# Optimization experiments

Measured on AMD Instinct MI355X. Metric: run time of the kernel, lower is better.

Reference implementation:

```python
import jax, jax.numpy as jnp
import numpy as np

H = 0.01          # implicit time step from __init__
KS = 1000.0       # spring stiffness
CG_ITERS = 30     # fixed CG iteration count
EPS = 1e-8


def setup_inputs() -> dict:
    key = jax.random.key(0)
    k1, k2, k3, k4 = jax.random.split(key, 4)
    NV, NE = 200000, 1200000
    rhs = jax.random.normal(k1, (NV, 3), dtype=jnp.float32)
    pos = jax.random.uniform(k2, (NV, 3), dtype=jnp.float32)
    mass = jnp.ones((NV,), dtype=jnp.float32)
    rest_len = jax.random.uniform(k3, (NE,), dtype=jnp.float32) * 0.5 + 0.1
    edges = jax.random.randint(k4, (NE, 2), 0, NV, dtype=jnp.int32)
    return {"rhs": rhs, "pos": pos, "mass": mass, "rest_len": rest_len, "edges": edges}


def _spring_jacobians(pos, edges, rest_len):
    # Per-spring force Jacobian df_i/dx_i for f_i = -ks (|d| - l0) d_hat, d = x_i - x_j
    d = pos[edges[:, 0]] - pos[edges[:, 1]]            # (NE, 3)
    l = jnp.sqrt(jnp.sum(d * d, axis=-1)) + EPS        # (NE,)
    dhat = d / l[:, None]
    ddT = dhat[:, :, None] * dhat[:, None, :]          # (NE, 3, 3)
    I3 = jnp.eye(3, dtype=pos.dtype)
    coef = (1.0 - rest_len / l)[:, None, None]
    Jx = -KS * (coef * (I3 - ddT) + ddT)               # negative semidefinite
    return Jx


def _matvec(v, Jx, e0, e1, mass):
    # A v = M v - h^2 (dF/dx) v, assembled over the spring graph
    dv_e = v[e0] - v[e1]                               # (NE, 3)
    f_e = jnp.einsum('eij,ej->ei', Jx, dv_e)           # (NE, 3)
    Jv = jnp.zeros_like(v).at[e0].add(f_e).at[e1].add(-f_e)
    return mass[:, None] * v - (H * H) * Jv


def reference(rhs, pos, mass, rest_len, edges):
    # Implicit mass-spring step: solve (M - h^2 J) dv = rhs with fixed-iteration CG
    Jx = _spring_jacobians(pos, edges, rest_len)
    e0, e1 = edges[:, 0], edges[:, 1]

    def matvec(v):
        return _matvec(v, Jx, e0, e1, mass)

    b = rhs
    x0 = jnp.zeros_like(b)                             # dv.fill(0.0)
    rs0 = jnp.vdot(b, b)

    def cg_step(carry, _):
        x, r, p, rs = carry
        Ap = matvec(p)
        alpha = rs / (jnp.vdot(p, Ap) + EPS)
        x = x + alpha * p
        r = r - alpha * Ap
        rs_new = jnp.vdot(r, r)
        p = r + (rs_new / (rs + EPS)) * p
        return (x, r, p, rs_new), None

    (x, _, _, _), _ = jax.lax.scan(cg_step, (x0, b, b, rs0), None, length=CG_ITERS)
    return x
```

## Files before the change

kernel.cpp:

```cpp
#include <hip/hip_runtime.h>

#define CG_ITERS 30
#define PAP_OFF 32
#define TILE 8192
#define CHAIN_TB 512
#define ROWSTRIDE 128

__device__ __forceinline__ float fadd32(float a, float b){ return __fadd_rn(a,b); }
__device__ __forceinline__ float fsub32(float a, float b){ return __fsub_rn(a,b); }
__device__ __forceinline__ float fmul32(float a, float b){ return __fmul_rn(a,b); }
__device__ __forceinline__ float fdiv32(float a, float b){ return __fdiv_rn(a,b); }

__device__ __forceinline__ void edge_force(int2 e, int eidx,
                                           const float* __restrict__ pos,
                                           const float* __restrict__ rl,
                                           const float* __restrict__ p,
                                           float f[3]) {
    int i0 = 3 * e.x, i1 = 3 * e.y;
    float d[3], dh[3], dv[3];
    d[0] = fsub32(pos[i0 + 0], pos[i1 + 0]);
    d[1] = fsub32(pos[i0 + 1], pos[i1 + 1]);
    d[2] = fsub32(pos[i0 + 2], pos[i1 + 2]);
    float ss = fadd32(fadd32(fmul32(d[0], d[0]), fmul32(d[1], d[1])), fmul32(d[2], d[2]));
    float l  = fadd32(__fsqrt_rn(ss), 1e-8f);
    dh[0] = fdiv32(d[0], l); dh[1] = fdiv32(d[1], l); dh[2] = fdiv32(d[2], l);
    float coef = fsub32(1.0f, fdiv32(rl[eidx], l));
    dv[0] = fsub32(p[i0 + 0], p[i1 + 0]);
    dv[1] = fsub32(p[i0 + 1], p[i1 + 1]);
    dv[2] = fsub32(p[i0 + 2], p[i1 + 2]);
    #pragma unroll
    for (int i = 0; i < 3; ++i) {
        float acc = 0.0f;
        #pragma unroll
        for (int j = 2; j >= 0; --j) {
            float dd = fmul32(dh[i], dh[j]);
            float t  = (i == j) ? fsub32(1.0f, dd) : fsub32(0.0f, dd);
            float w  = fadd32(fmul32(coef, t), dd);
            float Jx = fmul32(-1000.0f, w);
            acc = fadd32(acc, fmul32(Jx, dv[j]));
        }
        f[i] = acc;
    }
}

__global__ void count_k(const int2* __restrict__ ed, int* __restrict__ cnt0,
                        int* __restrict__ cnt1, int ne) {
    int i = blockIdx.x * blockDim.x + threadIdx.x;
    if (i >= ne) return;
    int2 e = ed[i];
    atomicAdd(&cnt0[e.x], 1);
    atomicAdd(&cnt1[e.y], 1);
}

__global__ void scan_k(const int* __restrict__ cnt0, const int* __restrict__ cnt1,
                       int* __restrict__ segoff, int* __restrict__ split,
                       int* __restrict__ cur0, int* __restrict__ cur1, int nv) {
    __shared__ int lds[1024];
    int tid = threadIdx.x;
    int chunk = (nv + 1023) / 1024;
    int lo = tid * chunk;
    int hi = lo + chunk; if (hi > nv) hi = nv; if (lo > nv) lo = nv;
    int s = 0;
    for (int v = lo; v < hi; ++v) s += cnt0[v] + cnt1[v];
    lds[tid] = s;
    __syncthreads();
    for (int off = 1; off < 1024; off <<= 1) {
        int t = (tid >= off) ? lds[tid - off] : 0;
        __syncthreads();
        lds[tid] += t;
        __syncthreads();
    }
    int run = lds[tid] - s;
    for (int v = lo; v < hi; ++v) {
        int c0 = cnt0[v], c1 = cnt1[v];
        segoff[v] = run;
        split[v]  = run + c0;
        cur0[v]   = run;
        cur1[v]   = run + c0;
        run += c0 + c1;
    }
    if (tid == 1023) segoff[nv] = lds[1023];
}

__global__ void fill_k(const int2* __restrict__ ed, int* __restrict__ cur0,
                       int* __restrict__ cur1, int* __restrict__ inc, int ne) {
    int i = blockIdx.x * blockDim.x + threadIdx.x;
    if (i >= ne) return;
    int2 e = ed[i];
    int s0 = atomicAdd(&cur0[e.x], 1); inc[s0] = i;
    int s1 = atomicAdd(&cur1[e.y], 1); inc[s1] = i;
}

__global__ void sort_k(int* __restrict__ inc, const int* __restrict__ segoff,
                       const int* __restrict__ split, int nv) {
    int v = blockIdx.x * blockDim.x + threadIdx.x;
    if (v >= nv) return;
    int lo = segoff[v], mid = split[v], hi = segoff[v + 1];
    for (int a = lo + 1; a < mid; ++a) {
        int key = inc[a]; int b = a - 1;
        while (b >= lo && inc[b] > key) { inc[b + 1] = inc[b]; --b; }
        inc[b + 1] = key;
    }
    for (int a = mid + 1; a < hi; ++a) {
        int key = inc[a]; int b = a - 1;
        while (b >= mid && inc[b] > key) { inc[b + 1] = inc[b]; --b; }
        inc[b + 1] = key;
    }
}

#define SCHED_FENCE() __builtin_amdgcn_sched_barrier(0)
#define ACC4(v) { s = fadd32(s, (v).x); s = fadd32(s, (v).y); \
                  s = fadd32(s, (v).z); s = fadd32(s, (v).w); }
#define G8_DECL(P) float4 P##0, P##1, P##2, P##3, P##4, P##5, P##6, P##7;
#define G8_LOAD(P, b4, base) { P##0=(b4)[(base)+0]; P##1=(b4)[(base)+1]; \
    P##2=(b4)[(base)+2]; P##3=(b4)[(base)+3]; P##4=(b4)[(base)+4]; \
    P##5=(b4)[(base)+5]; P##6=(b4)[(base)+6]; P##7=(b4)[(base)+7]; }
#define G8_ACC(P) { ACC4(P##0) ACC4(P##1) ACC4(P##2) ACC4(P##3) \
                    ACC4(P##4) ACC4(P##5) ACC4(P##6) ACC4(P##7) }

__device__ __forceinline__ void mark_range(int* __restrict__ tilecnt,
                                           int flo, int fhi) {
    if (fhi <= flo) return;
    __threadfence();
    int t0 = flo / TILE, t1 = (fhi - 1) / TILE;
    for (int t = t0; t <= t1; ++t) {
        int lo = t * TILE;       if (lo < flo) lo = flo;
        int hi = (t + 1) * TILE; if (hi > fhi) hi = fhi;
        atomicAdd(&tilecnt[t], hi - lo);
    }
}

__device__ void chain_consume(const float* __restrict__ prod,
                              int* __restrict__ tilecnt,
                              float* __restrict__ out, int n) {
    __shared__ float buf[2][TILE];
    __shared__ int sgen;
    int tid = threadIdx.x;
    int ntiles = (n + TILE - 1) / TILE;
    if (tid == 0) sgen = -1;
    __syncthreads();

#define WAITSTAGE(T) { \
        int lim = n - (T) * TILE; if (lim > TILE) lim = TILE; \
        if (tid == 64) { \
            while (__hip_atomic_load(&tilecnt[(T)], __ATOMIC_ACQUIRE, \
                                     __HIP_MEMORY_SCOPE_AGENT) < lim) \
                __builtin_amdgcn_s_sleep(1); \
            __hip_atomic_store(&sgen, (T), __ATOMIC_RELEASE, \
                               __HIP_MEMORY_SCOPE_WORKGROUP); \
        } \
        while (__hip_atomic_load(&sgen, __ATOMIC_ACQUIRE, \
                                 __HIP_MEMORY_SCOPE_WORKGROUP) < (T)) \
            __builtin_amdgcn_s_sleep(1); \
        float* dst = buf[(T) & 1]; \
        const float* src = prod + (size_t)(T) * TILE; \
        for (int i = tid - 64; i < lim; i += (CHAIN_TB - 64)) \
            dst[i] = __hip_atomic_load((const float*)&src[i], __ATOMIC_RELAXED, \
                                       __HIP_MEMORY_SCOPE_AGENT); \
    }

    if (tid >= 64) WAITSTAGE(0);
    __syncthreads();
    float s = 0.0f;
    for (int t = 0; t < ntiles; ++t) {
        if (t + 1 < ntiles && tid >= 64) WAITSTAGE(t + 1);
        if (tid == 0) {
            const float* b = buf[t & 1];
            int cfl = n - t * TILE; if (cfl > TILE) cfl = TILE;
            const float4* b4 = (const float4*)b;
            int c4 = cfl >> 2;
            int ng = c4 >> 3;
            int g = 0;
            if (ng >= 5) {
                G8_DECL(A) G8_DECL(B) G8_DECL(C)
                G8_LOAD(A, b4, 0)
                SCHED_FENCE();
                G8_LOAD(B, b4, 8)
                SCHED_FENCE();
                for (; g + 5 <= ng; g += 3) {
                    G8_LOAD(C, b4, (g + 2) << 3)  SCHED_FENCE();
                    G8_ACC(A)                     SCHED_FENCE();
                    G8_LOAD(A, b4, (g + 3) << 3)  SCHED_FENCE();
                    G8_ACC(B)                     SCHED_FENCE();
                    G8_LOAD(B, b4, (g + 4) << 3)  SCHED_FENCE();
                    G8_ACC(C)                     SCHED_FENCE();
                }
                G8_ACC(A)
                G8_ACC(B)
                g += 2;
            }
            for (; g < ng; ++g) {
                G8_DECL(D)
                G8_LOAD(D, b4, g << 3)
                G8_ACC(D)
            }
            for (int i2 = ng << 3; i2 < c4; ++i2) { float4 v = b4[i2]; ACC4(v) }
            for (int k2 = c4 << 2; k2 < cfl; ++k2) s = fadd32(s, b[k2]);
        }
        __syncthreads();
    }
    if (tid == 0) out[0] = s;
#undef WAITSTAGE
}


__global__ void __launch_bounds__(CHAIN_TB, 1)
initchain_k(const float* __restrict__ rhs, float* __restrict__ x,
            float* __restrict__ r, float* __restrict__ p,
            float* __restrict__ prod, int* __restrict__ tilecnt,
            float* __restrict__ out, int n) {
    if (blockIdx.x == 0) { chain_consume(prod, tilecnt, out, n); return; }
    int pb = blockIdx.x - 1;
    int j = pb * CHAIN_TB + threadIdx.x;
    if (j < n) {
        float b = rhs[j];
        x[j] = 0.0f; r[j] = b; p[j] = b;
        prod[j] = fmul32(b, b);
    }
    __syncthreads();
    if (threadIdx.x == 0) {
        int flo = pb * CHAIN_TB;
        int fhi = flo + CHAIN_TB; if (fhi > n) fhi = n;
        mark_range(tilecnt, flo, fhi);
    }
}

__global__ void __launch_bounds__(CHAIN_TB, 1)
mvchain_k(const int2* __restrict__ ed, const float* __restrict__ pos,
          const float* __restrict__ rl, const float* __restrict__ p,
          const float* __restrict__ mass, const int* __restrict__ inc,
          const int* __restrict__ segoff, const int* __restrict__ split,
          float* __restrict__ Ap, float* __restrict__ prod,
          int* __restrict__ tilecnt, float* __restrict__ out,
          int nv, int n3) {
    if (blockIdx.x == 0) { chain_consume(prod, tilecnt, out, n3); return; }
    int pb = blockIdx.x - 1;
    int v = pb * CHAIN_TB + threadIdx.x;
    if (v < nv) {
        int lo = segoff[v], mid = split[v], hi = segoff[v + 1];
        float a0 = 0.0f, a1 = 0.0f, a2 = 0.0f;
        for (int k = lo; k < mid; ++k) {
            int e = inc[k]; float f[3];
            edge_force(ed[e], e, pos, rl, p, f);
            a0 = fadd32(a0, f[0]); a1 = fadd32(a1, f[1]); a2 = fadd32(a2, f[2]);
        }
        for (int k = mid; k < hi; ++k) {
            int e = inc[k]; float f[3];
            edge_force(ed[e], e, pos, rl, p, f);
            a0 = fadd32(a0, -f[0]); a1 = fadd32(a1, -f[1]); a2 = fadd32(a2, -f[2]);
        }
        const float h2 = (float)(0.01 * 0.01);
        int j = 3 * v; float m = mass[v];
        float p0 = p[j], p1 = p[j + 1], p2 = p[j + 2];
        float A0 = fsub32(fmul32(m, p0), fmul32(h2, a0));
        float A1 = fsub32(fmul32(m, p1), fmul32(h2, a1));
        float A2 = fsub32(fmul32(m, p2), fmul32(h2, a2));
        Ap[j + 0] = A0; Ap[j + 1] = A1; Ap[j + 2] = A2;
        prod[j + 0] = fmul32(p0, A0);
        prod[j + 1] = fmul32(p1, A1);
        prod[j + 2] = fmul32(p2, A2);
    }
    __syncthreads();
    if (threadIdx.x == 0) {
        int vlo = pb * CHAIN_TB;
        int vhi = vlo + CHAIN_TB; if (vhi > nv) vhi = nv;
        mark_range(tilecnt, 3 * vlo, 3 * vhi);
    }
}

__global__ void __launch_bounds__(CHAIN_TB, 1)
xrchain_k(float* __restrict__ x, float* __restrict__ r,
          const float* __restrict__ p, const float* __restrict__ Ap,
          float* __restrict__ prod, const float* __restrict__ scal,
          int it, int* __restrict__ tilecnt, float* __restrict__ out,
          int do_chain, int n) {
    if (blockIdx.x == 0) {
        if (do_chain) chain_consume(prod, tilecnt, out, n);
        return;
    }
    int pb = blockIdx.x - 1;
    int j = pb * CHAIN_TB + threadIdx.x;
    if (j < n) {
        float alpha = (float)((double)scal[it] / ((double)scal[PAP_OFF + it] + 1e-8));
        x[j] = fadd32(x[j], fmul32(alpha, p[j]));
        float rn = fsub32(r[j], fmul32(alpha, Ap[j]));
        r[j] = rn;
        prod[j] = fmul32(rn, rn);
    }
    __syncthreads();
    if (threadIdx.x == 0) {
        int flo = pb * CHAIN_TB;
        int fhi = flo + CHAIN_TB; if (fhi > n) fhi = n;
        mark_range(tilecnt, flo, fhi);
    }
}

__global__ void __launch_bounds__(256)
p_k(const float* __restrict__ r, float* __restrict__ p,
    const float* __restrict__ scal, int it, int n) {
    int j = blockIdx.x * blockDim.x + threadIdx.x;
    if (j >= n) return;
    float beta = (float)((double)scal[it + 1] / ((double)scal[it] + 1e-8));
    p[j] = fadd32(r[j], fmul32(beta, p[j]));
}

extern "C" void kernel_launch(void* const* d_in, const int* in_sizes, int n_in,
                              void* d_out, int out_size, void* d_ws, size_t ws_size,
                              hipStream_t stream) {
    const float* rhs  = (const float*)d_in[0];
    const float* pos  = (const float*)d_in[1];
    const float* mass = (const float*)d_in[2];
    const float* rl   = (const float*)d_in[3];
    const int2*  ed   = (const int2*)d_in[4];
    float* x = (float*)d_out;

    int NV = in_sizes[0] / 3;
    int NE = in_sizes[3];
    int n3 = NV * 3;

    char* w = (char*)d_ws;
    float* r    = (float*)w;  w += (size_t)n3 * sizeof(float);
    float* p    = (float*)w;  w += (size_t)n3 * sizeof(float);
    float* Ap   = (float*)w;  w += (size_t)n3 * sizeof(float);
    float* prod = (float*)w;  w += (size_t)n3 * sizeof(float);
    int*   inc  = (int*)w;    w += (size_t)2 * NE * sizeof(int);
    int*   cnt0 = (int*)w;    w += (size_t)NV * sizeof(int);
    int*   cnt1 = (int*)w;    w += (size_t)NV * sizeof(int);
    int*   segoff = (int*)w;  w += (size_t)(NV + 1) * sizeof(int);
    int*   split  = (int*)w;  w += (size_t)NV * sizeof(int);
    int*   cur0   = (int*)w;  w += (size_t)NV * sizeof(int);
    int*   cur1   = (int*)w;  w += (size_t)NV * sizeof(int);
    float* scal    = (float*)w; w += (size_t)64 * sizeof(float);
    int*   tilecnt = (int*)w;

    hipMemsetAsync(cnt0, 0, (size_t)2 * NV * sizeof(int), stream);
    hipMemsetAsync(tilecnt, 0, (size_t)64 * ROWSTRIDE * sizeof(int), stream);

    const int tb = 256;
    int gE = (NE + tb - 1) / tb;
    int gV = (NV + tb - 1) / tb;
    int g3 = (n3 + tb - 1) / tb;

    int pV = (NV + CHAIN_TB - 1) / CHAIN_TB;
    int p3 = (n3 + CHAIN_TB - 1) / CHAIN_TB;

    count_k<<<gE, tb, 0, stream>>>(ed, cnt0, cnt1, NE);
    scan_k<<<1, 1024, 0, stream>>>(cnt0, cnt1, segoff, split, cur0, cur1, NV);
    fill_k<<<gE, tb, 0, stream>>>(ed, cur0, cur1, inc, NE);
    sort_k<<<gV, tb, 0, stream>>>(inc, segoff, split, NV);

    initchain_k<<<p3 + 1, CHAIN_TB, 0, stream>>>(rhs, x, r, p, prod,
                                                 tilecnt, &scal[0], n3);

    for (int it = 0; it < CG_ITERS; ++it) {
        mvchain_k<<<pV + 1, CHAIN_TB, 0, stream>>>(ed, pos, rl, p, mass, inc,
                                                   segoff, split, Ap, prod,
                                                   tilecnt + (size_t)(1 + it) * ROWSTRIDE,
                                                   &scal[PAP_OFF + it], NV, n3);
        int doch = (it + 1 < CG_ITERS) ? 1 : 0;
        xrchain_k<<<p3 + 1, CHAIN_TB, 0, stream>>>(x, r, p, Ap, prod, scal, it,
                                                   tilecnt + (size_t)(32 + it) * ROWSTRIDE,
                                                   &scal[it + 1], doch, n3);
        if (doch) {
            p_k<<<g3, tb, 0, stream>>>(r, p, scal, it, n3);
        }
    }
}
```

Before: 105.4 ms.

## Fuse p-update into matvec gather and use single-block xr reduction kernels

The separate p = r + beta*p kernel is removed. The matvec now computes p on the fly from r and the previous p, using ping-pong p buffers, and writes the new p for each owned vertex. The multi-block x/r update plus chain-consumer kernels are replaced by single-block kernels, in which 448 threads do the elementwise update into shared tiles while one thread keeps the ordered serial sum. The aim is fewer launches and no cross-block tile handshaking. The cost is that every edge gather now reads r as well as p, and the elementwise work runs on a single CU.

```diff
diff --git a/kernel.cpp b/kernel.cpp
--- a/kernel.cpp
+++ b/kernel.cpp
@@ -3,6 +3,7 @@
 #define CG_ITERS 30
 #define PAP_OFF 32
 #define TILE 8192
+#define TILEB 16384
 #define CHAIN_TB 512
 #define ROWSTRIDE 128
 
@@ -11,10 +12,18 @@
 __device__ __forceinline__ float fmul32(float a, float b){ return __fmul_rn(a,b); }
 __device__ __forceinline__ float fdiv32(float a, float b){ return __fdiv_rn(a,b); }
 
+__device__ __forceinline__ float pval(const float* r, const float* ps,
+                                      float beta, int use_beta, int idx) {
+    float pv = ps[idx];
+    if (use_beta) pv = fadd32(r[idx], fmul32(beta, pv));
+    return pv;
+}
+
 __device__ __forceinline__ void edge_force(int2 e, int eidx,
                                            const float* __restrict__ pos,
                                            const float* __restrict__ rl,
-                                           const float* __restrict__ p,
+                                           const float* r, const float* ps,
+                                           float beta, int use_beta,
                                            float f[3]) {
     int i0 = 3 * e.x, i1 = 3 * e.y;
     float d[3], dh[3], dv[3];
@@ -25,9 +34,9 @@
     float l  = fadd32(__fsqrt_rn(ss), 1e-8f);
     dh[0] = fdiv32(d[0], l); dh[1] = fdiv32(d[1], l); dh[2] = fdiv32(d[2], l);
     float coef = fsub32(1.0f, fdiv32(rl[eidx], l));
-    dv[0] = fsub32(p[i0 + 0], p[i1 + 0]);
-    dv[1] = fsub32(p[i0 + 1], p[i1 + 1]);
-    dv[2] = fsub32(p[i0 + 2], p[i1 + 2]);
+    dv[0] = fsub32(pval(r, ps, beta, use_beta, i0 + 0), pval(r, ps, beta, use_beta, i1 + 0));
+    dv[1] = fsub32(pval(r, ps, beta, use_beta, i0 + 1), pval(r, ps, beta, use_beta, i1 + 1));
+    dv[2] = fsub32(pval(r, ps, beta, use_beta, i0 + 2), pval(r, ps, beta, use_beta, i1 + 2));
     #pragma unroll
     for (int i = 0; i < 3; ++i) {
         float acc = 0.0f;
@@ -117,6 +126,39 @@
     P##5=(b4)[(base)+5]; P##6=(b4)[(base)+6]; P##7=(b4)[(base)+7]; }
 #define G8_ACC(P) { ACC4(P##0) ACC4(P##1) ACC4(P##2) ACC4(P##3) \
                     ACC4(P##4) ACC4(P##5) ACC4(P##6) ACC4(P##7) }
+
+__device__ __forceinline__ void chain_tile(const float* __restrict__ b,
+                                           int cfl, float& s) {
+    const float4* b4 = (const float4*)b;
+    int c4 = cfl >> 2;
+    int ng = c4 >> 3;
+    int g = 0;
+    if (ng >= 5) {
+        G8_DECL(A) G8_DECL(B) G8_DECL(C)
+        G8_LOAD(A, b4, 0)
+        SCHED_FENCE();
+        G8_LOAD(B, b4, 8)
+        SCHED_FENCE();
+        for (; g + 5 <= ng; g += 3) {
+            G8_LOAD(C, b4, (g + 2) << 3)  SCHED_FENCE();
+            G8_ACC(A)                     SCHED_FENCE();
+            G8_LOAD(A, b4, (g + 3) << 3)  SCHED_FENCE();
+            G8_ACC(B)                     SCHED_FENCE();
+            G8_LOAD(B, b4, (g + 4) << 3)  SCHED_FENCE();
+            G8_ACC(C)                     SCHED_FENCE();
+        }
+        G8_ACC(A)
+        G8_ACC(B)
+        g += 2;
+    }
+    for (; g < ng; ++g) {
+        G8_DECL(D)
+        G8_LOAD(D, b4, g << 3)
+        G8_ACC(D)
+    }
+    for (int i2 = ng << 3; i2 < c4; ++i2) { float4 v = b4[i2]; ACC4(v) }
+    for (int k2 = c4 << 2; k2 < cfl; ++k2) s = fadd32(s, b[k2]);
+}
 
 __device__ __forceinline__ void mark_range(int* __restrict__ tilecnt,
                                            int flo, int fhi) {
@@ -165,37 +207,8 @@
     for (int t = 0; t < ntiles; ++t) {
         if (t + 1 < ntiles && tid >= 64) WAITSTAGE(t + 1);
         if (tid == 0) {
-            const float* b = buf[t & 1];
             int cfl = n - t * TILE; if (cfl > TILE) cfl = TILE;
-            const float4* b4 = (const float4*)b;
-            int c4 = cfl >> 2;
-            int ng = c4 >> 3;
-            int g = 0;
-            if (ng >= 5) {
-                G8_DECL(A) G8_DECL(B) G8_DECL(C)
-                G8_LOAD(A, b4, 0)
-                SCHED_FENCE();
-                G8_LOAD(B, b4, 8)
-                SCHED_FENCE();
-                for (; g + 5 <= ng; g += 3) {
-                    G8_LOAD(C, b4, (g + 2) << 3)  SCHED_FENCE();
-                    G8_ACC(A)                     SCHED_FENCE();
-                    G8_LOAD(A, b4, (g + 3) << 3)  SCHED_FENCE();
-                    G8_ACC(B)                     SCHED_FENCE();
-                    G8_LOAD(B, b4, (g + 4) << 3)  SCHED_FENCE();
-                    G8_ACC(C)                     SCHED_FENCE();
-                }
-                G8_ACC(A)
-                G8_ACC(B)
-                g += 2;
-            }
-            for (; g < ng; ++g) {
-                G8_DECL(D)
-                G8_LOAD(D, b4, g << 3)
-                G8_ACC(D)
-            }
-            for (int i2 = ng << 3; i2 < c4; ++i2) { float4 v = b4[i2]; ACC4(v) }
-            for (int k2 = c4 << 2; k2 < cfl; ++k2) s = fadd32(s, b[k2]);
+            chain_tile(buf[t & 1], cfl, s);
         }
         __syncthreads();
     }
@@ -203,55 +216,41 @@
 #undef WAITSTAGE
 }
 
-
-__global__ void __launch_bounds__(CHAIN_TB, 1)
-initchain_k(const float* __restrict__ rhs, float* __restrict__ x,
-            float* __restrict__ r, float* __restrict__ p,
-            float* __restrict__ prod, int* __restrict__ tilecnt,
-            float* __restrict__ out, int n) {
-    if (blockIdx.x == 0) { chain_consume(prod, tilecnt, out, n); return; }
-    int pb = blockIdx.x - 1;
-    int j = pb * CHAIN_TB + threadIdx.x;
-    if (j < n) {
-        float b = rhs[j];
-        x[j] = 0.0f; r[j] = b; p[j] = b;
-        prod[j] = fmul32(b, b);
-    }
-    __syncthreads();
-    if (threadIdx.x == 0) {
-        int flo = pb * CHAIN_TB;
-        int fhi = flo + CHAIN_TB; if (fhi > n) fhi = n;
-        mark_range(tilecnt, flo, fhi);
-    }
-}
-
 __global__ void __launch_bounds__(CHAIN_TB, 1)
 mvchain_k(const int2* __restrict__ ed, const float* __restrict__ pos,
-          const float* __restrict__ rl, const float* __restrict__ p,
+          const float* __restrict__ rl, const float* __restrict__ r,
+          const float* p_src, float* p_dst,
           const float* __restrict__ mass, const int* __restrict__ inc,
           const int* __restrict__ segoff, const int* __restrict__ split,
           float* __restrict__ Ap, float* __restrict__ prod,
           int* __restrict__ tilecnt, float* __restrict__ out,
+          const float* __restrict__ scal, int it, int use_beta,
           int nv, int n3) {
     if (blockIdx.x == 0) { chain_consume(prod, tilecnt, out, n3); return; }
     int pb = blockIdx.x - 1;
     int v = pb * CHAIN_TB + threadIdx.x;
     if (v < nv) {
+        float beta = 0.0f;
+        if (use_beta)
+            beta = (float)((double)scal[it] / ((double)scal[it - 1] + 1e-8));
         int lo = segoff[v], mid = split[v], hi = segoff[v + 1];
         float a0 = 0.0f, a1 = 0.0f, a2 = 0.0f;
         for (int k = lo; k < mid; ++k) {
             int e = inc[k]; float f[3];
-            edge_force(ed[e], e, pos, rl, p, f);
+            edge_force(ed[e], e, pos, rl, r, p_src, beta, use_beta, f);
             a0 = fadd32(a0, f[0]); a1 = fadd32(a1, f[1]); a2 = fadd32(a2, f[2]);
         }
         for (int k = mid; k < hi; ++k) {
             int e = inc[k]; float f[3];
-            edge_force(ed[e], e, pos, rl, p, f);
+            edge_force(ed[e], e, pos, rl, r, p_src, beta, use_beta, f);
             a0 = fadd32(a0, -f[0]); a1 = fadd32(a1, -f[1]); a2 = fadd32(a2, -f[2]);
         }
         const float h2 = (float)(0.01 * 0.01);
         int j = 3 * v; float m = mass[v];
-        float p0 = p[j], p1 = p[j + 1], p2 = p[j + 2];
+        float p0 = pval(r, p_src, beta, use_beta, j + 0);
+        float p1 = pval(r, p_src, beta, use_beta, j + 1);
+        float p2 = pval(r, p_src, beta, use_beta, j + 2);
+        if (use_beta) { p_dst[j] = p0; p_dst[j + 1] = p1; p_dst[j + 2] = p2; }
         float A0 = fsub32(fmul32(m, p0), fmul32(h2, a0));
         float A1 = fsub32(fmul32(m, p1), fmul32(h2, a1));
         float A2 = fsub32(fmul32(m, p2), fmul32(h2, a2));
@@ -268,40 +267,102 @@
     }
 }
 
+
 __global__ void __launch_bounds__(CHAIN_TB, 1)
-xrchain_k(float* __restrict__ x, float* __restrict__ r,
-          const float* __restrict__ p, const float* __restrict__ Ap,
-          float* __restrict__ prod, const float* __restrict__ scal,
-          int it, int* __restrict__ tilecnt, float* __restrict__ out,
-          int do_chain, int n) {
-    if (blockIdx.x == 0) {
-        if (do_chain) chain_consume(prod, tilecnt, out, n);
-        return;
-    }
-    int pb = blockIdx.x - 1;
-    int j = pb * CHAIN_TB + threadIdx.x;
-    if (j < n) {
-        float alpha = (float)((double)scal[it] / ((double)scal[PAP_OFF + it] + 1e-8));
-        x[j] = fadd32(x[j], fmul32(alpha, p[j]));
-        float rn = fsub32(r[j], fmul32(alpha, Ap[j]));
-        r[j] = rn;
-        prod[j] = fmul32(rn, rn);
-    }
-    __syncthreads();
-    if (threadIdx.x == 0) {
-        int flo = pb * CHAIN_TB;
-        int fhi = flo + CHAIN_TB; if (fhi > n) fhi = n;
-        mark_range(tilecnt, flo, fhi);
-    }
+initrs_k(const float* __restrict__ rhs, float* __restrict__ x,
+         float* __restrict__ r, float* __restrict__ p,
+         float* __restrict__ out, int n) {
+    __shared__ float buf[2][TILEB];
+    int tid = threadIdx.x;
+    int ntiles = (n + TILEB - 1) / TILEB;
+    const float4* b4g = (const float4*)rhs;
+    float4* x4 = (float4*)x; float4* r4 = (float4*)r; float4* p4 = (float4*)p;
+
+#define STAGE_INIT(T) { \
+        int lim = n - (T) * TILEB; if (lim > TILEB) lim = TILEB; \
+        int nf4 = lim >> 2; int base4 = (T) * (TILEB >> 2); \
+        float4* d4 = (float4*)buf[(T) & 1]; \
+        for (int i4 = tid - 64; i4 < nf4; i4 += (CHAIN_TB - 64)) { \
+            float4 bv = b4g[base4 + i4]; \
+            float4 z; z.x = 0.0f; z.y = 0.0f; z.z = 0.0f; z.w = 0.0f; \
+            float4 pr; \
+            pr.x = fmul32(bv.x, bv.x); pr.y = fmul32(bv.y, bv.y); \
+            pr.z = fmul32(bv.z, bv.z); pr.w = fmul32(bv.w, bv.w); \
+            x4[base4 + i4] = z; r4[base4 + i4] = bv; p4[base4 + i4] = bv; \
+            d4[i4] = pr; \
+        } }
+
+    if (tid >= 64) STAGE_INIT(0);
+    __syncthreads();
+    float s = 0.0f;
+    for (int t = 0; t < ntiles; ++t) {
+        if (t + 1 < ntiles && tid >= 64) STAGE_INIT(t + 1);
+        if (tid == 0) {
+            int cfl = n - t * TILEB; if (cfl > TILEB) cfl = TILEB;
+            chain_tile(buf[t & 1], cfl, s);
+        }
+        __syncthreads();
+    }
+    if (tid == 0) out[0] = s;
+#undef STAGE_INIT
+}
+
+__global__ void __launch_bounds__(CHAIN_TB, 1)
+xrrs_k(float* __restrict__ x, float* __restrict__ r,
+       const float* __restrict__ p, const float* __restrict__ Ap,
+       const float* __restrict__ scal, int it,
+       float* __restrict__ out, int n) {
+    __shared__ float buf[2][TILEB];
+    int tid = threadIdx.x;
+    int ntiles = (n + TILEB - 1) / TILEB;
+    float alpha = (float)((double)scal[it] / ((double)scal[PAP_OFF + it] + 1e-8));
+    float4* x4 = (float4*)x; float4* r4 = (float4*)r;
+    const float4* p4 = (const float4*)p; const float4* a4 = (const float4*)Ap;
+
+#define STAGE_XR(T) { \
+        int lim = n - (T) * TILEB; if (lim > TILEB) lim = TILEB; \
+        int nf4 = lim >> 2; int base4 = (T) * (TILEB >> 2); \
+        float4* d4 = (float4*)buf[(T) & 1]; \
+        for (int i4 = tid - 64; i4 < nf4; i4 += (CHAIN_TB - 64)) { \
+            float4 xv = x4[base4 + i4]; float4 rv = r4[base4 + i4]; \
+            float4 pv = p4[base4 + i4]; float4 av = a4[base4 + i4]; \
+            float4 xn, rn, pr; \
+            xn.x = fadd32(xv.x, fmul32(alpha, pv.x)); \
+            xn.y = fadd32(xv.y, fmul32(alpha, pv.y)); \
+            xn.z = fadd32(xv.z, fmul32(alpha, pv.z)); \
+            xn.w = fadd32(xv.w, fmul32(alpha, pv.w)); \
+            rn.x = fsub32(rv.x, fmul32(alpha, av.x)); \
+            rn.y = fsub32(rv.y, fmul32(alpha, av.y)); \
+            rn.z = fsub32(rv.z, fmul32(alpha, av.z)); \
+            rn.w = fsub32(rv.w, fmul32(alpha, av.w)); \
+            pr.x = fmul32(rn.x, rn.x); pr.y = fmul32(rn.y, rn.y); \
+            pr.z = fmul32(rn.z, rn.z); pr.w = fmul32(rn.w, rn.w); \
+            x4[base4 + i4] = xn; r4[base4 + i4] = rn; \
+            d4[i4] = pr; \
+        } }
+
+    if (tid >= 64) STAGE_XR(0);
+    __syncthreads();
+    float s = 0.0f;
+    for (int t = 0; t < ntiles; ++t) {
+        if (t + 1 < ntiles && tid >= 64) STAGE_XR(t + 1);
+        if (tid == 0) {
+            int cfl = n - t * TILEB; if (cfl > TILEB) cfl = TILEB;
+            chain_tile(buf[t & 1], cfl, s);
+        }
+        __syncthreads();
+    }
+    if (tid == 0) out[0] = s;
+#undef STAGE_XR
 }
 
 __global__ void __launch_bounds__(256)
-p_k(const float* __restrict__ r, float* __restrict__ p,
-    const float* __restrict__ scal, int it, int n) {
+xfin_k(float* __restrict__ x, const float* __restrict__ p,
+       const float* __restrict__ scal, int it, int n) {
     int j = blockIdx.x * blockDim.x + threadIdx.x;
     if (j >= n) return;
-    float beta = (float)((double)scal[it + 1] / ((double)scal[it] + 1e-8));
-    p[j] = fadd32(r[j], fmul32(beta, p[j]));
+    float alpha = (float)((double)scal[it] / ((double)scal[PAP_OFF + it] + 1e-8));
+    x[j] = fadd32(x[j], fmul32(alpha, p[j]));
 }
 
 extern "C" void kernel_launch(void* const* d_in, const int* in_sizes, int n_in,
@@ -320,7 +381,8 @@
 
     char* w = (char*)d_ws;
     float* r    = (float*)w;  w += (size_t)n3 * sizeof(float);
-    float* p    = (float*)w;  w += (size_t)n3 * sizeof(float);
+    float* pA   = (float*)w;  w += (size_t)n3 * sizeof(float);
+    float* pB   = (float*)w;  w += (size_t)n3 * sizeof(float);
     float* Ap   = (float*)w;  w += (size_t)n3 * sizeof(float);
     float* prod = (float*)w;  w += (size_t)n3 * sizeof(float);
     int*   inc  = (int*)w;    w += (size_t)2 * NE * sizeof(int);
@@ -340,29 +402,35 @@
     int gE = (NE + tb - 1) / tb;
     int gV = (NV + tb - 1) / tb;
     int g3 = (n3 + tb - 1) / tb;
-
     int pV = (NV + CHAIN_TB - 1) / CHAIN_TB;
-    int p3 = (n3 + CHAIN_TB - 1) / CHAIN_TB;
 
     count_k<<<gE, tb, 0, stream>>>(ed, cnt0, cnt1, NE);
     scan_k<<<1, 1024, 0, stream>>>(cnt0, cnt1, segoff, split, cur0, cur1, NV);
     fill_k<<<gE, tb, 0, stream>>>(ed, cur0, cur1, inc, NE);
     sort_k<<<gV, tb, 0, stream>>>(inc, segoff, split, NV);
 
-    initchain_k<<<p3 + 1, CHAIN_TB, 0, stream>>>(rhs, x, r, p, prod,
-                                                 tilecnt, &scal[0], n3);
+    initrs_k<<<1, CHAIN_TB, 0, stream>>>(rhs, x, r, pA, &scal[0], n3);
 
     for (int it = 0; it < CG_ITERS; ++it) {
-        mvchain_k<<<pV + 1, CHAIN_TB, 0, stream>>>(ed, pos, rl, p, mass, inc,
-                                                   segoff, split, Ap, prod,
+        const float* psrc; float* pdst; const float* puse;
+        int use_beta = (it > 0);
+        if (it == 0) { psrc = pA; pdst = pA; puse = pA; }
+        else {
+            psrc = (it & 1) ? pA : pB;
+            pdst = (it & 1) ? pB : pA;
+            puse = pdst;
+        }
+        mvchain_k<<<pV + 1, CHAIN_TB, 0, stream>>>(ed, pos, rl, r, psrc, pdst,
+                                                   mass, inc, segoff, split,
+                                                   Ap, prod,
                                                    tilecnt + (size_t)(1 + it) * ROWSTRIDE,
-                                                   &scal[PAP_OFF + it], NV, n3);
-        int doch = (it + 1 < CG_ITERS) ? 1 : 0;
-        xrchain_k<<<p3 + 1, CHAIN_TB, 0, stream>>>(x, r, p, Ap, prod, scal, it,
-                                                   tilecnt + (size_t)(32 + it) * ROWSTRIDE,
-                                                   &scal[it + 1], doch, n3);
-        if (doch) {
-            p_k<<<g3, tb, 0, stream>>>(r, p, scal, it, n3);
-        }
-    }
-}
+                                                   &scal[PAP_OFF + it], scal,
+                                                   it, use_beta, NV, n3);
+        if (it + 1 < CG_ITERS) {
+            xrrs_k<<<1, CHAIN_TB, 0, stream>>>(x, r, puse, Ap, scal, it,
+                                               &scal[it + 1], n3);
+        } else {
+            xfin_k<<<g3, tb, 0, stream>>>(x, puse, scal, it, n3);
+        }
+    }
+}
```

Result: no change. 106.5 ms (+1.0%).
